# Kernel optimization log

Measured on AMD Instinct MI355X. Metric: run time of the kernel, lower is better.

## Reference

```python
import jax, jax.numpy as jnp
import numpy as np

B, S, D = 2, 4096, 512
H = 8
HD = D // H  # 64


def setup_inputs() -> dict:
    key = jax.random.key(0)
    ks = jax.random.split(key, 9)
    sc = 1.0 / np.sqrt(D)
    inp = {
        "x": jax.random.normal(ks[0], (B, S, D), dtype=jnp.float32),
        "W_q": jax.random.normal(ks[1], (D, D), dtype=jnp.float32) * sc,
        "b_q": jax.random.normal(ks[2], (D,), dtype=jnp.float32) * 0.01,
        "W_k": jax.random.normal(ks[3], (D, D), dtype=jnp.float32) * sc,
        "b_k": jax.random.normal(ks[4], (D,), dtype=jnp.float32) * 0.01,
        "W_v": jax.random.normal(ks[5], (D, D), dtype=jnp.float32) * sc,
        "b_v": jax.random.normal(ks[6], (D,), dtype=jnp.float32) * 0.01,
        "W_o": jax.random.normal(ks[7], (D, D), dtype=jnp.float32) * sc,
        "b_o": jax.random.normal(ks[8], (D,), dtype=jnp.float32) * 0.01,
    }
    return inp


def reference(x, W_q, b_q, W_k, b_k, W_v, b_v, W_o, b_o):
    # QKV projections (torch Linear: x @ W.T + b)
    q = x @ W_q.T + b_q  # [B,S,D]
    k = x @ W_k.T + b_k
    v = x @ W_v.T + b_v
    # split heads -> [B,H,S,HD]
    def split(t):
        return t.reshape(B, S, H, HD).transpose(0, 2, 1, 3)
    q, k, v = split(q), split(k), split(v)
    scale = 1.0 / jnp.sqrt(jnp.float32(HD))
    scores = jnp.einsum("bhsd,bhtd->bhst", q, k) * scale  # [B,H,S,S]
    weights = jax.nn.softmax(scores, axis=-1)
    attn = jnp.einsum("bhst,bhtd->bhsd", weights, v)  # [B,H,S,HD]
    attn = attn.transpose(0, 2, 1, 3).reshape(B, S, D)
    return attn @ W_o.T + b_o
```

## Files before the change

### kernel.cpp

```cpp
#include <hip/hip_runtime.h>
#include <hip/hip_bf16.h>
#include <stdint.h>


typedef __attribute__((ext_vector_type(8))) short short8;
typedef __attribute__((ext_vector_type(4))) short sv4;
typedef __attribute__((ext_vector_type(4))) float floatx4;

#define MFMA(a, b, c) __builtin_amdgcn_mfma_f32_16x16x32_bf16((a), (b), (c), 0, 0, 0)

typedef __attribute__((address_space(1))) const void* gas_t;
typedef __attribute__((address_space(3))) void* las_t;
#define GLDS16(g, l) __builtin_amdgcn_global_load_lds((gas_t)(g), (las_t)(l), 16, 0, 0)

#define SM_SHIFT 13.0f

__device__ __forceinline__ float fexp2(float x) {
#if __has_builtin(__builtin_amdgcn_exp2f)
    return __builtin_amdgcn_exp2f(x);
#else
    float r;
    asm("v_exp_f32 %0, %1" : "=v"(r) : "v"(x));
    return r;
#endif
}

__device__ __forceinline__ short f2bf(float f) {
    union { float f; uint32_t u; } c; c.f = f;
    uint32_t u = c.u;
    u += 0x7fffu + ((u >> 16) & 1u);
    return (short)(u >> 16);
}
__device__ __forceinline__ float bf2f(short s) {
    union { float f; uint32_t u; } c; c.u = ((uint32_t)(uint16_t)s) << 16;
    return c.f;
}
__device__ __forceinline__ int pack2(float a, float b) {
    return (int)(uint16_t)f2bf(a) | ((int)(uint16_t)f2bf(b) << 16);
}
__device__ __forceinline__ int pack2rn(float a, float b) {
#if __has_builtin(__builtin_amdgcn_cvt_pk_bf16_f32)
    auto r = __builtin_amdgcn_cvt_pk_bf16_f32(a, b);
    int out; __builtin_memcpy(&out, &r, 4);
    return out;
#else
    int r;
    asm("v_cvt_pk_bf16_f32 %0, %1, %2" : "=v"(r) : "v"(a), "v"(b));
    return r;
#endif
}

__global__ void cvt_all(const float* __restrict__ x,
                        const float* __restrict__ wq, const float* __restrict__ wk,
                        const float* __restrict__ wv, const float* __restrict__ wo,
                        short* __restrict__ xb, short* __restrict__ wqb,
                        short* __restrict__ wkb, short* __restrict__ wvb,
                        short* __restrict__ wohi, short* __restrict__ wolo)
{
    int bid = blockIdx.x;
    if (bid < 2048) {
        int i = (bid * 256 + threadIdx.x) * 8;
        floatx4 v0 = *(const floatx4*)(x + i);
        floatx4 v1 = *(const floatx4*)(x + i + 4);
        short8 o;
        #pragma unroll
        for (int j = 0; j < 4; ++j) { o[j] = f2bf(v0[j]); o[4 + j] = f2bf(v1[j]); }
        *(short8*)(xb + i) = o;
    } else if (bid < 2432) {
        int idx = (bid - 2048) * 256 + threadIdx.x;
        int which = idx >> 15;
        int i = (idx & 32767) * 8;
        const float* src = which == 0 ? wq : which == 1 ? wk : wv;
        short* dst = which == 0 ? wqb : which == 1 ? wkb : wvb;
        floatx4 v0 = *(const floatx4*)(src + i);
        floatx4 v1 = *(const floatx4*)(src + i + 4);
        short8 o;
        #pragma unroll
        for (int j = 0; j < 4; ++j) { o[j] = f2bf(v0[j]); o[4 + j] = f2bf(v1[j]); }
        *(short8*)(dst + i) = o;
    } else {
        int i = ((bid - 2432) * 256 + threadIdx.x) * 8;
        floatx4 v0 = *(const floatx4*)(wo + i);
        floatx4 v1 = *(const floatx4*)(wo + i + 4);
        short8 h, l;
        #pragma unroll
        for (int j = 0; j < 4; ++j) {
            short hh = f2bf(v0[j]); h[j] = hh; l[j] = f2bf(v0[j] - bf2f(hh));
            short hh1 = f2bf(v1[j]); h[4 + j] = hh1; l[4 + j] = f2bf(v1[j] - bf2f(hh1));
        }
        *(short8*)(wohi + i) = h;
        *(short8*)(wolo + i) = l;
    }
}

__global__ __launch_bounds__(256) void qkv_gemm(
    const short* __restrict__ Xb,
    const short* __restrict__ Wq, const short* __restrict__ Wk, const short* __restrict__ Wv,
    const float* __restrict__ bq, const float* __restrict__ bk, const float* __restrict__ bv,
    short* __restrict__ Qo, short* __restrict__ Ko, short* __restrict__ VTo)
{
    __shared__ short SMEM[16384];
    #define ASH(bf) (SMEM + (bf) * 4096)
    #define BSH(bf) (SMEM + 8192 + (bf) * 4096)
    const int lane = threadIdx.x & 63, wave = threadIdx.x >> 6;
    const int col = lane & 15, quad = lane >> 4;
    const int wm = wave & 1, wn = wave >> 1;
    const int m0 = blockIdx.x * 128;
    const int by = blockIdx.y;
    const int which = by >> 2;
    const int n0 = (by & 3) * 128;
    const short* W = which == 0 ? Wq : which == 1 ? Wk : Wv;
    const float* bias = which == 0 ? bq : which == 1 ? bk : bv;
    const float oscale = which == 0 ? 0.1803368801111204f : 1.0f;

    const int rl = lane >> 2, pch = lane & 3;
    const int lch = pch ^ (rl & 3) ^ ((rl >> 2) & 3);
    const int seg = wave * 2;
    const short* ag0 = Xb + (size_t)(m0 + seg * 16 + rl) * 512 + lch * 8;
    const short* ag1 = ag0 + (size_t)16 * 512;
    const short* bg0 = W + (size_t)(n0 + seg * 16 + rl) * 512 + lch * 8;
    const short* bg1 = bg0 + (size_t)16 * 512;

    floatx4 acc[4][4] = {};

    GLDS16(ag0, ASH(0) + seg * 512);
    GLDS16(ag1, ASH(0) + (seg + 1) * 512);
    GLDS16(bg0, BSH(0) + seg * 512);
    GLDS16(bg1, BSH(0) + (seg + 1) * 512);
    __syncthreads();

    for (int t = 0; t < 16; ++t) {
        const int cur = t & 1;
        if (t < 15) {
            const int kb = (t + 1) * 32;
            GLDS16(ag0 + kb, ASH(cur ^ 1) + seg * 512);
            GLDS16(ag1 + kb, ASH(cur ^ 1) + (seg + 1) * 512);
            GLDS16(bg0 + kb, BSH(cur ^ 1) + seg * 512);
            GLDS16(bg1 + kb, BSH(cur ^ 1) + (seg + 1) * 512);
        }
        short8 af[4], bf[4];
        #pragma unroll
        for (int it = 0; it < 4; ++it) {
            const int rA = wm * 64 + it * 16 + col;
            const int pA = quad ^ (rA & 3) ^ ((rA >> 2) & 3);
            af[it] = *(const short8*)(ASH(cur) + rA * 32 + pA * 8);
            const int rB = wn * 64 + it * 16 + col;
            const int pB = quad ^ (rB & 3) ^ ((rB >> 2) & 3);
            bf[it] = *(const short8*)(BSH(cur) + rB * 32 + pB * 8);
        }
        #pragma unroll
        for (int i = 0; i < 4; ++i)
            #pragma unroll
            for (int j = 0; j < 4; ++j)
                acc[i][j] = MFMA(af[i], bf[j], acc[i][j]);
        __syncthreads();
    }

    if (which < 2) {
        #pragma unroll
        for (int i = 0; i < 4; ++i)
            #pragma unroll
            for (int j = 0; j < 4; ++j)
                #pragma unroll
                for (int r = 0; r < 4; ++r) {
                    int m = m0 + wm * 64 + i * 16 + quad * 4 + r;
                    int n = n0 + wn * 64 + j * 16 + col;
                    float v = (acc[i][j][r] + bias[n]) * oscale;
                    int b = m >> 12, s = m & 4095;
                    int h = n >> 6, hd = n & 63;
                    int bh = b * 8 + h;
                    short bv16 = f2bf(v);
                    if (which == 0) Qo[((size_t)bh * 4096 + s) * 64 + hd] = bv16;
                    else            Ko[((size_t)bh * 4096 + s) * 64 + hd] = bv16;
                }
    } else {
        short* tb = SMEM + wave * 4096;
        #pragma unroll
        for (int n2 = 0; n2 < 2; ++n2) {
            #pragma unroll
            for (int jj = 0; jj < 2; ++jj) {
                const int j = n2 * 2 + jj;
                const int n_rel = jj * 16 + col;
                const float bv_ = bias[n0 + wn * 64 + j * 16 + col];
                #pragma unroll
                for (int i = 0; i < 4; ++i) {
                    const int m_rel = i * 16 + quad * 4;
                    *(int*)(tb + n_rel * 72 + m_rel) =
                        pack2(acc[i][j][0] + bv_, acc[i][j][1] + bv_);
                    *(int*)(tb + n_rel * 72 + m_rel + 2) =
                        pack2(acc[i][j][2] + bv_, acc[i][j][3] + bv_);
                }
            }
            asm volatile("s_waitcnt lgkmcnt(0)" ::: "memory");
            const int n_rel = lane & 31, half = lane >> 5;
            const int n = n0 + wn * 64 + n2 * 32 + n_rel;
            const int h = n >> 6, hd = n & 63;
            const int bh = (m0 >> 12) * 8 + h;
            const int s0 = (m0 & 4095) + wm * 64 + half * 32;
            const short* src = tb + n_rel * 72 + half * 32;
            short* dst = VTo + ((size_t)bh * 64 + hd) * 4096 + s0;
            #pragma unroll
            for (int qq = 0; qq < 4; ++qq) {
                union { sv4 hh[2]; int4 v; } u;
                u.hh[0] = *(const sv4*)(src + 4 * qq);
                u.hh[1] = *(const sv4*)(src + 16 + 4 * qq);
                *(int4*)(dst + qq * 8) = u.v;
            }
        }
    }
    #undef ASH
    #undef BSH
}

__global__ __launch_bounds__(512, 2) void flash_attn(
    const short* __restrict__ Q, const short* __restrict__ Kk,
    const short* __restrict__ VT,
    short* __restrict__ Ahi, short* __restrict__ Alo)
{
    __shared__ float SMEMf[16384];
    short* SMEM = (short*)SMEMf;
    const int lane = threadIdx.x & 63, wave = threadIdx.x >> 6;
    const int col = lane & 15, quad = lane >> 4;
    const int id = blockIdx.x;
    const int bh = id & 15;
    const int bx = id >> 4;
    const int b = bh >> 3, h = bh & 7;
    const int qw = wave & 3, kz = wave >> 2;
    const int q0 = bx * 256 + qw * 64;
    const int kbeg = kz * 2048;
    const size_t base = (size_t)bh * 4096 * 64;
    const size_t vbase = (size_t)bh * 64 * 4096;

    short8 qf0[4], qf1[4];
    #pragma unroll
    for (int qt = 0; qt < 4; ++qt) {
        const short* qp = Q + base + (size_t)(q0 + qt * 16 + col) * 64 + quad * 8;
        qf0[qt] = *(const short8*)(qp);
        qf1[qt] = *(const short8*)(qp + 32);
    }

    const int rloc = lane >> 3, pch = lane & 7;
    const int lch = pch ^ rloc;
    const short* kst0 = Kk + base + (size_t)(kbeg + qw * 16 + rloc) * 64 + lch * 8;
    const short* kst1 = kst0 + (size_t)8 * 64;
    const short* vst0 = VT + vbase + (size_t)(qw * 16 + rloc) * 4096 + kbeg + lch * 8;
    const short* vst1 = vst0 + (size_t)8 * 4096;

    floatx4 o[4][4] = {};
    floatx4 lacc[4] = {};
    const floatx4 mshift = {-SM_SHIFT, -SM_SHIFT, -SM_SHIFT, -SM_SHIFT};
    short8 ones8;
    #pragma unroll
    for (int j = 0; j < 8; ++j) ones8[j] = (short)0x3F80;

    const int sw = col & 7;
    const int co0 = (quad ^ sw) * 8;
    const int co1 = ((quad + 4) ^ sw) * 8;
    const short* kb0 = SMEM + kz * 8192 + col * 64 + co0;
    const short* kb1 = SMEM + kz * 8192 + col * 64 + co1;
    const short* vb0 = SMEM + 16384 + kz * 8192 + col * 64 + co0;
    const short* vb1 = SMEM + 16384 + kz * 8192 + col * 64 + co1;
    short* const klds0 = SMEM + kz * 8192 + qw * 1024;
    short* const klds1 = klds0 + 4096;
    short* const vlds0 = SMEM + 16384 + kz * 8192 + qw * 1024;
    short* const vlds1 = vlds0 + 4096;

    GLDS16(kst0, klds0);
    GLDS16(kst1, klds0 + 512);
    GLDS16(vst0, vlds0);
    GLDS16(vst1, vlds0 + 512);
    __syncthreads();

#define FA_BODY(CUR, KO2, PF)                                                  \
    {                                                                          \
        if (PF) {                                                              \
            GLDS16(kst0 + (size_t)(KO2) * 64, (CUR) ? klds0 : klds1);          \
            GLDS16(kst1 + (size_t)(KO2) * 64, ((CUR) ? klds0 : klds1) + 512);  \
            GLDS16(vst0 + (KO2), (CUR) ? vlds0 : vlds1);                       \
            GLDS16(vst1 + (KO2), ((CUR) ? vlds0 : vlds1) + 512);               \
        }                                                                      \
        _Pragma("unroll")                                                      \
        for (int c = 0; c < 2; ++c) {                                          \
            short8 k0a = *(const short8*)(kb0 + (CUR) * 4096 + (2 * c) * 1024);     \
            short8 k1a = *(const short8*)(kb1 + (CUR) * 4096 + (2 * c) * 1024);     \
            short8 k0b = *(const short8*)(kb0 + (CUR) * 4096 + (2 * c + 1) * 1024); \
            short8 k1b = *(const short8*)(kb1 + (CUR) * 4096 + (2 * c + 1) * 1024); \
            floatx4 saA[4], saB[4];                                            \
            __builtin_amdgcn_s_setprio(1);                                     \
            _Pragma("unroll")                                                  \
            for (int qt = 0; qt < 4; ++qt) {                                   \
                floatx4 z = MFMA(k0a, qf0[qt], mshift);                        \
                saA[qt] = MFMA(k1a, qf1[qt], z);                               \
                floatx4 z2 = MFMA(k0b, qf0[qt], mshift);                       \
                saB[qt] = MFMA(k1b, qf1[qt], z2);                              \
            }                                                                  \
            __builtin_amdgcn_s_setprio(0);                                     \
            short8 pb[4];                                                      \
            _Pragma("unroll")                                                  \
            for (int qt = 0; qt < 4; ++qt) {                                   \
                union { int i[4]; short8 s; } u;                               \
                u.i[0] = pack2rn(fexp2(saA[qt][0]), fexp2(saA[qt][1]));        \
                u.i[1] = pack2rn(fexp2(saA[qt][2]), fexp2(saA[qt][3]));        \
                u.i[2] = pack2rn(fexp2(saB[qt][0]), fexp2(saB[qt][1]));        \
                u.i[3] = pack2rn(fexp2(saB[qt][2]), fexp2(saB[qt][3]));        \
                pb[qt] = u.s;                                                  \
                lacc[qt] = MFMA(ones8, u.s, lacc[qt]);                         \
            }                                                                  \
            __builtin_amdgcn_s_setprio(1);                                     \
            _Pragma("unroll")                                                  \
            for (int mt = 0; mt < 4; ++mt) {                                   \
                const short8 vv = *(const short8*)(((c) ? vb1 : vb0) + (CUR) * 4096 + mt * 1024); \
                o[0][mt] = MFMA(vv, pb[0], o[0][mt]);                          \
                o[1][mt] = MFMA(vv, pb[1], o[1][mt]);                          \
                o[2][mt] = MFMA(vv, pb[2], o[2][mt]);                          \
                o[3][mt] = MFMA(vv, pb[3], o[3][mt]);                          \
            }                                                                  \
            __builtin_amdgcn_s_setprio(0);                                     \
        }                                                                      \
        __syncthreads();                                                       \
    }

    int ko2 = 64;
    for (int t2 = 0; t2 < 15; ++t2) {
        FA_BODY(0, ko2, 1); ko2 += 64;
        FA_BODY(1, ko2, 1); ko2 += 64;
    }
    FA_BODY(0, ko2, 1);
    FA_BODY(1, 0, 0);
#undef FA_BODY

    float* Osh = SMEMf;
    float* Msh = SMEMf + 8704;
    #pragma unroll
    for (int p = 0; p < 2; ++p) {
        const int ta = 2 * p, tb_ = 2 * p + 1;
        if (kz == 1) {
            #pragma unroll
            for (int mt = 0; mt < 4; ++mt) {
                *(floatx4*)&Osh[(qw * 2 + 0) * 1088 + col * 68 + mt * 16 + quad * 4] = o[ta][mt];
                *(floatx4*)&Osh[(qw * 2 + 1) * 1088 + col * 68 + mt * 16 + quad * 4] = o[tb_][mt];
            }
            if (quad == 0) {
                Msh[qw * 32 + col] = lacc[ta][0];
                Msh[qw * 32 + col + 16] = lacc[tb_][0];
            }
        }
        __syncthreads();
        if (kz == 0) {
            float linvA = 1.0f / (lacc[ta][0] + Msh[qw * 32 + col]);
            float linvB = 1.0f / (lacc[tb_][0] + Msh[qw * 32 + col + 16]);
            size_t rowA = (size_t)(b * 4096 + q0 + ta * 16 + col) * 512 + h * 64;
            size_t rowB = rowA + (size_t)16 * 512;
            #pragma unroll
            for (int mt = 0; mt < 4; ++mt) {
                floatx4 o2A = *(const floatx4*)&Osh[(qw * 2 + 0) * 1088 + col * 68 + mt * 16 + quad * 4];
                floatx4 o2B = *(const floatx4*)&Osh[(qw * 2 + 1) * 1088 + col * 68 + mt * 16 + quad * 4];
                float w0 = (o[ta][mt][0] + o2A[0]) * linvA;
                float w1 = (o[ta][mt][1] + o2A[1]) * linvA;
                float w2 = (o[ta][mt][2] + o2A[2]) * linvA;
                float w3 = (o[ta][mt][3] + o2A[3]) * linvA;
                int2 hi, lo;
                hi.x = pack2(w0, w1); hi.y = pack2(w2, w3);
                lo.x = pack2(w0 - bf2f(f2bf(w0)), w1 - bf2f(f2bf(w1)));
                lo.y = pack2(w2 - bf2f(f2bf(w2)), w3 - bf2f(f2bf(w3)));
                *(int2*)(Ahi + rowA + mt * 16 + quad * 4) = hi;
                *(int2*)(Alo + rowA + mt * 16 + quad * 4) = lo;
                w0 = (o[tb_][mt][0] + o2B[0]) * linvB;
                w1 = (o[tb_][mt][1] + o2B[1]) * linvB;
                w2 = (o[tb_][mt][2] + o2B[2]) * linvB;
                w3 = (o[tb_][mt][3] + o2B[3]) * linvB;
                hi.x = pack2(w0, w1); hi.y = pack2(w2, w3);
                lo.x = pack2(w0 - bf2f(f2bf(w0)), w1 - bf2f(f2bf(w1)));
                lo.y = pack2(w2 - bf2f(f2bf(w2)), w3 - bf2f(f2bf(w3)));
                *(int2*)(Ahi + rowB + mt * 16 + quad * 4) = hi;
                *(int2*)(Alo + rowB + mt * 16 + quad * 4) = lo;
            }
        }
        __syncthreads();
    }
}

__global__ __launch_bounds__(256) void out_gemm(
    const short* __restrict__ Ahi, const short* __restrict__ Alo,
    const short* __restrict__ Whi, const short* __restrict__ Wlo,
    const float* __restrict__ bo, float* __restrict__ Out)
{
    __shared__ short SMEM[24576];
    #define AHS(bf) (SMEM + (bf) * 4096)
    #define ALS(bf) (SMEM + 8192 + (bf) * 4096)
    #define BHS(bf) (SMEM + 16384 + (bf) * 2048)
    #define BLS(bf) (SMEM + 20480 + (bf) * 2048)
    const int lane = threadIdx.x & 63, wave = threadIdx.x >> 6;
    const int col = lane & 15, quad = lane >> 4;
    const int wm = wave & 1, wn = wave >> 1;
    const int m0 = blockIdx.x * 128;
    const int n0 = blockIdx.y * 64;

    const int rl = lane >> 2, pch = lane & 3;
    const int lch = pch ^ (rl & 3) ^ ((rl >> 2) & 3);
    const int seg = wave * 2;
    const short* ah0 = Ahi + (size_t)(m0 + seg * 16 + rl) * 512 + lch * 8;
    const short* ah1 = ah0 + (size_t)16 * 512;
    const short* al0 = Alo + (size_t)(m0 + seg * 16 + rl) * 512 + lch * 8;
    const short* al1 = al0 + (size_t)16 * 512;
    const short* bh0 = Whi + (size_t)(n0 + wave * 16 + rl) * 512 + lch * 8;
    const short* bl0 = Wlo + (size_t)(n0 + wave * 16 + rl) * 512 + lch * 8;

    floatx4 acc[4][2] = {};

    GLDS16(ah0, AHS(0) + seg * 512);
    GLDS16(ah1, AHS(0) + (seg + 1) * 512);
    GLDS16(al0, ALS(0) + seg * 512);
    GLDS16(al1, ALS(0) + (seg + 1) * 512);
    GLDS16(bh0, BHS(0) + wave * 512);
    GLDS16(bl0, BLS(0) + wave * 512);
    __syncthreads();

    for (int t = 0; t < 16; ++t) {
        const int cur = t & 1;
        if (t < 15) {
            const int kb = (t + 1) * 32;
            GLDS16(ah0 + kb, AHS(cur ^ 1) + seg * 512);
            GLDS16(ah1 + kb, AHS(cur ^ 1) + (seg + 1) * 512);
            GLDS16(al0 + kb, ALS(cur ^ 1) + seg * 512);
            GLDS16(al1 + kb, ALS(cur ^ 1) + (seg + 1) * 512);
            GLDS16(bh0 + kb, BHS(cur ^ 1) + wave * 512);
            GLDS16(bl0 + kb, BLS(cur ^ 1) + wave * 512);
        }
        short8 ahf[4], alf[4], bhf[2], blf[2];
        #pragma unroll
        for (int it = 0; it < 4; ++it) {
            const int rA = wm * 64 + it * 16 + col;
            const int pA = quad ^ (rA & 3) ^ ((rA >> 2) & 3);
            ahf[it] = *(const short8*)(AHS(cur) + rA * 32 + pA * 8);
            alf[it] = *(const short8*)(ALS(cur) + rA * 32 + pA * 8);
        }
        #pragma unroll
        for (int jt = 0; jt < 2; ++jt) {
            const int rB = wn * 32 + jt * 16 + col;
            const int pB = quad ^ (rB & 3) ^ ((rB >> 2) & 3);
            bhf[jt] = *(const short8*)(BHS(cur) + rB * 32 + pB * 8);
            blf[jt] = *(const short8*)(BLS(cur) + rB * 32 + pB * 8);
        }
        #pragma unroll
        for (int i = 0; i < 4; ++i)
            #pragma unroll
            for (int j = 0; j < 2; ++j) {
                acc[i][j] = MFMA(ahf[i], bhf[j], acc[i][j]);
                acc[i][j] = MFMA(ahf[i], blf[j], acc[i][j]);
                acc[i][j] = MFMA(alf[i], bhf[j], acc[i][j]);
            }
        __syncthreads();
    }

    #pragma unroll
    for (int i = 0; i < 4; ++i)
        #pragma unroll
        for (int j = 0; j < 2; ++j)
            #pragma unroll
            for (int r = 0; r < 4; ++r) {
                int m = m0 + wm * 64 + i * 16 + quad * 4 + r;
                int n = n0 + wn * 32 + j * 16 + col;
                Out[(size_t)m * 512 + n] = acc[i][j][r] + bo[n];
            }
    #undef AHS
    #undef ALS
    #undef BHS
    #undef BLS
}

extern "C" void kernel_launch(void* const* d_in, const int* in_sizes, int n_in,
                              void* d_out, int out_size, void* d_ws, size_t ws_size,
                              hipStream_t stream) {
    (void)in_sizes; (void)n_in; (void)out_size; (void)ws_size;
    const float* x   = (const float*)d_in[0];
    const float* W_q = (const float*)d_in[1];
    const float* b_q = (const float*)d_in[2];
    const float* W_k = (const float*)d_in[3];
    const float* b_k = (const float*)d_in[4];
    const float* W_v = (const float*)d_in[5];
    const float* b_v = (const float*)d_in[6];
    const float* W_o = (const float*)d_in[7];
    const float* b_o = (const float*)d_in[8];
    float* out = (float*)d_out;
    char* ws = (char*)d_ws;

    short* Xb   = (short*)(ws + 0);
    short* Wqb  = (short*)(ws + 8388608);
    short* Wkb  = (short*)(ws + 8912896);
    short* Wvb  = (short*)(ws + 9437184);
    short* Wohi = (short*)(ws + 9961472);
    short* Wolo = (short*)(ws + 10485760);
    short* Qb   = (short*)(ws + 11010048);
    short* Kb   = (short*)(ws + 19398656);
    short* VTb  = (short*)(ws + 27787264);
    short* Ahi  = (short*)(ws + 36175872);
    short* Alo  = (short*)(ws + 44564480);

    cvt_all<<<dim3(2560), dim3(256), 0, stream>>>(x, W_q, W_k, W_v, W_o,
                                                  Xb, Wqb, Wkb, Wvb, Wohi, Wolo);
    qkv_gemm<<<dim3(64, 12), dim3(256), 0, stream>>>(Xb, Wqb, Wkb, Wvb, b_q, b_k, b_v, Qb, Kb, VTb);
    flash_attn<<<dim3(256), dim3(512), 0, stream>>>(Qb, Kb, VTb, Ahi, Alo);
    out_gemm<<<dim3(64, 8), dim3(256), 0, stream>>>(Ahi, Alo, Wohi, Wolo, b_o, out);
}
```

Before: 184.5 us.

## Halve per-wave query tile in flash attention to double grid and occupancy

Each wave now handles 32 query rows instead of 64, so each block covers 128 queries and the grid doubles to 512 blocks. Launch bounds are raised to 4 blocks per CU to allow more waves per SIMD, and the accumulator and register arrays shrink to match. The epilogue loses its two-pass loop. The aim is to fill all CUs with 512 blocks and hide latency through occupancy, at the cost of loading each K/V tile twice as often per query and doing fewer MFMAs per LDS K/V read. The 64 KB static LDS per block may keep the 4-blocks-per-CU target from being reached.

```diff
diff --git a/kernel.cpp b/kernel.cpp
--- a/kernel.cpp
+++ b/kernel.cpp
@@ -212,7 +212,7 @@
     #undef BSH
 }
 
-__global__ __launch_bounds__(512, 2) void flash_attn(
+__global__ __launch_bounds__(512, 4) void flash_attn(
     const short* __restrict__ Q, const short* __restrict__ Kk,
     const short* __restrict__ VT,
     short* __restrict__ Ahi, short* __restrict__ Alo)
@@ -226,14 +226,14 @@
     const int bx = id >> 4;
     const int b = bh >> 3, h = bh & 7;
     const int qw = wave & 3, kz = wave >> 2;
-    const int q0 = bx * 256 + qw * 64;
+    const int q0 = bx * 128 + qw * 32;
     const int kbeg = kz * 2048;
     const size_t base = (size_t)bh * 4096 * 64;
     const size_t vbase = (size_t)bh * 64 * 4096;
 
-    short8 qf0[4], qf1[4];
+    short8 qf0[2], qf1[2];
     #pragma unroll
-    for (int qt = 0; qt < 4; ++qt) {
+    for (int qt = 0; qt < 2; ++qt) {
         const short* qp = Q + base + (size_t)(q0 + qt * 16 + col) * 64 + quad * 8;
         qf0[qt] = *(const short8*)(qp);
         qf1[qt] = *(const short8*)(qp + 32);
@@ -246,8 +246,8 @@
     const short* vst0 = VT + vbase + (size_t)(qw * 16 + rloc) * 4096 + kbeg + lch * 8;
     const short* vst1 = vst0 + (size_t)8 * 4096;
 
-    floatx4 o[4][4] = {};
-    floatx4 lacc[4] = {};
+    floatx4 o[2][4] = {};
+    floatx4 lacc[2] = {};
     const floatx4 mshift = {-SM_SHIFT, -SM_SHIFT, -SM_SHIFT, -SM_SHIFT};
     short8 ones8;
     #pragma unroll
@@ -285,19 +285,19 @@
             short8 k1a = *(const short8*)(kb1 + (CUR) * 4096 + (2 * c) * 1024);     \
             short8 k0b = *(const short8*)(kb0 + (CUR) * 4096 + (2 * c + 1) * 1024); \
             short8 k1b = *(const short8*)(kb1 + (CUR) * 4096 + (2 * c + 1) * 1024); \
-            floatx4 saA[4], saB[4];                                            \
+            floatx4 saA[2], saB[2];                                            \
             __builtin_amdgcn_s_setprio(1);                                     \
             _Pragma("unroll")                                                  \
-            for (int qt = 0; qt < 4; ++qt) {                                   \
+            for (int qt = 0; qt < 2; ++qt) {                                   \
                 floatx4 z = MFMA(k0a, qf0[qt], mshift);                        \
                 saA[qt] = MFMA(k1a, qf1[qt], z);                               \
                 floatx4 z2 = MFMA(k0b, qf0[qt], mshift);                       \
                 saB[qt] = MFMA(k1b, qf1[qt], z2);                              \
             }                                                                  \
             __builtin_amdgcn_s_setprio(0);                                     \
-            short8 pb[4];                                                      \
+            short8 pb[2];                                                      \
             _Pragma("unroll")                                                  \
-            for (int qt = 0; qt < 4; ++qt) {                                   \
+            for (int qt = 0; qt < 2; ++qt) {                                   \
                 union { int i[4]; short8 s; } u;                               \
                 u.i[0] = pack2rn(fexp2(saA[qt][0]), fexp2(saA[qt][1]));        \
                 u.i[1] = pack2rn(fexp2(saA[qt][2]), fexp2(saA[qt][3]));        \
@@ -312,8 +312,6 @@
                 const short8 vv = *(const short8*)(((c) ? vb1 : vb0) + (CUR) * 4096 + mt * 1024); \
                 o[0][mt] = MFMA(vv, pb[0], o[0][mt]);                          \
                 o[1][mt] = MFMA(vv, pb[1], o[1][mt]);                          \
-                o[2][mt] = MFMA(vv, pb[2], o[2][mt]);                          \
-                o[3][mt] = MFMA(vv, pb[3], o[3][mt]);                          \
             }                                                                  \
             __builtin_amdgcn_s_setprio(0);                                     \
         }                                                                      \
@@ -331,52 +329,47 @@
 
     float* Osh = SMEMf;
     float* Msh = SMEMf + 8704;
-    #pragma unroll
-    for (int p = 0; p < 2; ++p) {
-        const int ta = 2 * p, tb_ = 2 * p + 1;
-        if (kz == 1) {
-            #pragma unroll
-            for (int mt = 0; mt < 4; ++mt) {
-                *(floatx4*)&Osh[(qw * 2 + 0) * 1088 + col * 68 + mt * 16 + quad * 4] = o[ta][mt];
-                *(floatx4*)&Osh[(qw * 2 + 1) * 1088 + col * 68 + mt * 16 + quad * 4] = o[tb_][mt];
-            }
-            if (quad == 0) {
-                Msh[qw * 32 + col] = lacc[ta][0];
-                Msh[qw * 32 + col + 16] = lacc[tb_][0];
-            }
-        }
-        __syncthreads();
-        if (kz == 0) {
-            float linvA = 1.0f / (lacc[ta][0] + Msh[qw * 32 + col]);
-            float linvB = 1.0f / (lacc[tb_][0] + Msh[qw * 32 + col + 16]);
-            size_t rowA = (size_t)(b * 4096 + q0 + ta * 16 + col) * 512 + h * 64;
-            size_t rowB = rowA + (size_t)16 * 512;
-            #pragma unroll
-            for (int mt = 0; mt < 4; ++mt) {
-                floatx4 o2A = *(const floatx4*)&Osh[(qw * 2 + 0) * 1088 + col * 68 + mt * 16 + quad * 4];
-                floatx4 o2B = *(const floatx4*)&Osh[(qw * 2 + 1) * 1088 + col * 68 + mt * 16 + quad * 4];
-                float w0 = (o[ta][mt][0] + o2A[0]) * linvA;
-                float w1 = (o[ta][mt][1] + o2A[1]) * linvA;
-                float w2 = (o[ta][mt][2] + o2A[2]) * linvA;
-                float w3 = (o[ta][mt][3] + o2A[3]) * linvA;
-                int2 hi, lo;
-                hi.x = pack2(w0, w1); hi.y = pack2(w2, w3);
-                lo.x = pack2(w0 - bf2f(f2bf(w0)), w1 - bf2f(f2bf(w1)));
-                lo.y = pack2(w2 - bf2f(f2bf(w2)), w3 - bf2f(f2bf(w3)));
-                *(int2*)(Ahi + rowA + mt * 16 + quad * 4) = hi;
-                *(int2*)(Alo + rowA + mt * 16 + quad * 4) = lo;
-                w0 = (o[tb_][mt][0] + o2B[0]) * linvB;
-                w1 = (o[tb_][mt][1] + o2B[1]) * linvB;
-                w2 = (o[tb_][mt][2] + o2B[2]) * linvB;
-                w3 = (o[tb_][mt][3] + o2B[3]) * linvB;
-                hi.x = pack2(w0, w1); hi.y = pack2(w2, w3);
-                lo.x = pack2(w0 - bf2f(f2bf(w0)), w1 - bf2f(f2bf(w1)));
-                lo.y = pack2(w2 - bf2f(f2bf(w2)), w3 - bf2f(f2bf(w3)));
-                *(int2*)(Ahi + rowB + mt * 16 + quad * 4) = hi;
-                *(int2*)(Alo + rowB + mt * 16 + quad * 4) = lo;
-            }
-        }
-        __syncthreads();
+    if (kz == 1) {
+        #pragma unroll
+        for (int mt = 0; mt < 4; ++mt) {
+            *(floatx4*)&Osh[(qw * 2 + 0) * 1088 + col * 68 + mt * 16 + quad * 4] = o[0][mt];
+            *(floatx4*)&Osh[(qw * 2 + 1) * 1088 + col * 68 + mt * 16 + quad * 4] = o[1][mt];
+        }
+        if (quad == 0) {
+            Msh[qw * 32 + col] = lacc[0][0];
+            Msh[qw * 32 + col + 16] = lacc[1][0];
+        }
+    }
+    __syncthreads();
+    if (kz == 0) {
+        float linvA = 1.0f / (lacc[0][0] + Msh[qw * 32 + col]);
+        float linvB = 1.0f / (lacc[1][0] + Msh[qw * 32 + col + 16]);
+        size_t rowA = (size_t)(b * 4096 + q0 + col) * 512 + h * 64;
+        size_t rowB = rowA + (size_t)16 * 512;
+        #pragma unroll
+        for (int mt = 0; mt < 4; ++mt) {
+            floatx4 o2A = *(const floatx4*)&Osh[(qw * 2 + 0) * 1088 + col * 68 + mt * 16 + quad * 4];
+            floatx4 o2B = *(const floatx4*)&Osh[(qw * 2 + 1) * 1088 + col * 68 + mt * 16 + quad * 4];
+            float w0 = (o[0][mt][0] + o2A[0]) * linvA;
+            float w1 = (o[0][mt][1] + o2A[1]) * linvA;
+            float w2 = (o[0][mt][2] + o2A[2]) * linvA;
+            float w3 = (o[0][mt][3] + o2A[3]) * linvA;
+            int2 hi, lo;
+            hi.x = pack2(w0, w1); hi.y = pack2(w2, w3);
+            lo.x = pack2(w0 - bf2f(f2bf(w0)), w1 - bf2f(f2bf(w1)));
+            lo.y = pack2(w2 - bf2f(f2bf(w2)), w3 - bf2f(f2bf(w3)));
+            *(int2*)(Ahi + rowA + mt * 16 + quad * 4) = hi;
+            *(int2*)(Alo + rowA + mt * 16 + quad * 4) = lo;
+            w0 = (o[1][mt][0] + o2B[0]) * linvB;
+            w1 = (o[1][mt][1] + o2B[1]) * linvB;
+            w2 = (o[1][mt][2] + o2B[2]) * linvB;
+            w3 = (o[1][mt][3] + o2B[3]) * linvB;
+            hi.x = pack2(w0, w1); hi.y = pack2(w2, w3);
+            lo.x = pack2(w0 - bf2f(f2bf(w0)), w1 - bf2f(f2bf(w1)));
+            lo.y = pack2(w2 - bf2f(f2bf(w2)), w3 - bf2f(f2bf(w3)));
+            *(int2*)(Ahi + rowB + mt * 16 + quad * 4) = hi;
+            *(int2*)(Alo + rowB + mt * 16 + quad * 4) = lo;
+        }
     }
 }
 
@@ -500,6 +493,6 @@
     cvt_all<<<dim3(2560), dim3(256), 0, stream>>>(x, W_q, W_k, W_v, W_o,
                                                   Xb, Wqb, Wkb, Wvb, Wohi, Wolo);
     qkv_gemm<<<dim3(64, 12), dim3(256), 0, stream>>>(Xb, Wqb, Wkb, Wvb, b_q, b_k, b_v, Qb, Kb, VTb);
-    flash_attn<<<dim3(256), dim3(512), 0, stream>>>(Qb, Kb, VTb, Ahi, Alo);
+    flash_attn<<<dim3(512), dim3(512), 0, stream>>>(Qb, Kb, VTb, Ahi, Alo);
     out_gemm<<<dim3(64, 8), dim3(256), 0, stream>>>(Ahi, Alo, Wohi, Wolo, b_o, out);
 }
```

Measured after the change: 190.5 us. +3.3%, slower.
